# Performance work log

Hardware: AMD Instinct MI355X
Metric: run time of the kernel (lower is better)

## Reference

```python
import jax, jax.numpy as jnp
import numpy as np

THRESHOLD = 1.0
DECAY = 0.9
SURR_SLOPE = 10.0

B, T, IN, HID, OUT = 1024, 16, 2312, 1024, 10


def setup_inputs() -> dict:
    key = jax.random.key(0)
    kx, kw1, kb1, kw2, kb2 = jax.random.split(key, 5)
    x = jax.random.normal(kx, (B, T, IN), dtype=jnp.float32)
    # PyTorch nn.Linear default init: U(-1/sqrt(fan_in), 1/sqrt(fan_in))
    lim1 = 1.0 / np.sqrt(IN)
    lim2 = 1.0 / np.sqrt(HID)
    W1 = jax.random.uniform(kw1, (HID, IN), jnp.float32, -lim1, lim1)
    b1 = jax.random.uniform(kb1, (HID,), jnp.float32, -lim1, lim1)
    W2 = jax.random.uniform(kw2, (OUT, HID), jnp.float32, -lim2, lim2)
    b2 = jax.random.uniform(kb2, (OUT,), jnp.float32, -lim2, lim2)
    return {"x": x, "W1": W1, "b1": b1, "W2": W2, "b2": b2}


def _lif_step(v, inp):
    # leaky integrate-and-fire with sigmoid surrogate spike
    v_new = DECAY * v + inp
    spike = jax.nn.sigmoid(SURR_SLOPE * (v_new - THRESHOLD))
    v_next = v_new * (1.0 - spike)
    return v_next, spike


def reference(x, W1, b1, W2, b2):
    # x: [B, T, IN] -> spikes: [B, T, OUT]
    Bn = x.shape[0]
    v1_0 = jnp.zeros((Bn, W1.shape[0]), x.dtype)
    v2_0 = jnp.zeros((Bn, W2.shape[0]), x.dtype)

    # Precompute the first linear over all time steps (batched GEMM).
    h_all = jnp.einsum('bti,hi->bth', x, W1) + b1  # [B, T, HID]

    def step(carry, h_t):
        v1, v2 = carry
        v1, s1 = _lif_step(v1, h_t)                 # [B, HID]
        o_t = s1 @ W2.T + b2                        # [B, OUT]
        v2, s2 = _lif_step(v2, o_t)
        return (v1, v2), s2

    h_tb = jnp.swapaxes(h_all, 0, 1)                # [T, B, HID]
    _, spikes = jax.lax.scan(step, (v1_0, v2_0), h_tb)
    return jnp.swapaxes(spikes, 0, 1)               # [B, T, OUT]
```

## Files before the change

### kernel.cpp

```cpp
#include <hip/hip_runtime.h>

typedef _Float16 half8  __attribute__((ext_vector_type(8)));
typedef _Float16 half4v __attribute__((ext_vector_type(4)));
typedef float    floatx4 __attribute__((ext_vector_type(4)));

#define K_DIM 2312
#define KP    2368
#define N_DIM 1024
#define M_DIM 16384
#define T_DIM 16
#define O_DIM 10
#define NKT   73
#define NT_OLD 73
#define LDP 40

__global__ __launch_bounds__(256) void cvt_f32_f16_pad(const float* __restrict__ src,
                                                       _Float16* __restrict__ dst) {
  int row = blockIdx.x;
  const float* s = src + (size_t)row * K_DIM;
  _Float16* d = dst + (size_t)row * KP;
  for (int c = threadIdx.x; c < 296; c += 256) {
    half8 o;
    if (c < 289) {
      floatx4 a = *(const floatx4*)(s + c * 8);
      floatx4 b = *(const floatx4*)(s + c * 8 + 4);
      #pragma unroll
      for (int e = 0; e < 4; ++e) { o[e] = (_Float16)a[e]; o[4 + e] = (_Float16)b[e]; }
    } else {
      o = half8{0, 0, 0, 0, 0, 0, 0, 0};
    }
    *(half8*)(d + c * 8) = o;
  }
}

__device__ __forceinline__ void gload16(const void* g, void* l) {
  __builtin_amdgcn_global_load_lds((const __attribute__((address_space(1))) void*)g,
                                   (__attribute__((address_space(3))) void*)l, 16, 0, 0);
}

#define VMCNT(n)  asm volatile("s_waitcnt vmcnt(" #n ")" ::: "memory")
#define SBAR      __builtin_amdgcn_sched_barrier(0)

__global__ __launch_bounds__(512, 2) void gemm_fused3(const float* __restrict__ X,
                                                      const _Float16* __restrict__ Bw,
                                                      const float* __restrict__ b1,
                                                      float* __restrict__ h) {
  __shared__ __align__(16) float    As[3][256 * 32];
  __shared__ __align__(16) _Float16 Bs[3][256 * 32];

  const int tid  = threadIdx.x;
  const int lane = tid & 63;
  const int w    = tid >> 6;
  const int wm   = (w >> 1) * 64;
  const int wn   = (w & 1) * 128;
  const int bm   = blockIdx.x & 63;
  const int bn   = blockIdx.x >> 6;
  const int m0   = bm * 256;
  const int n0   = bn * 256;

  const int rOffA = lane >> 3;
  const int gsrcA = (lane & 7) ^ (lane >> 3);
  const float* xaw = X + (size_t)(m0 + w * 32) * K_DIM;

  const int rlo  = lane >> 2;
  const int keyB = (rlo >> 1) & 3;
  const int cch  = (lane & 3) ^ keyB;
  const _Float16* bg = Bw + (size_t)(n0 + w * 32 + rlo) * KP + cch * 8;
  const int stbB = (w * 32) * 32;

  floatx4 acc[4][8];
  #pragma unroll
  for (int i = 0; i < 4; ++i)
    #pragma unroll
    for (int j = 0; j < 8; ++j)
      acc[i][j] = floatx4{0.f, 0.f, 0.f, 0.f};

  const int fr = lane & 15;
  const int q  = lane >> 4;
  const int rdsB = (q ^ ((fr >> 1) & 3)) * 8;
  int offB[8];
  #pragma unroll
  for (int j = 0; j < 8; ++j) offB[j] = (wn + j * 16 + fr) * 32 + rdsB;
  const int cA = fr & 7;
  int offA0[4], offA1[4];
  #pragma unroll
  for (int i = 0; i < 4; ++i) {
    const int rowA = wm + i * 16 + fr;
    offA0[i] = rowA * 32 + ((2 * q)     ^ cA) * 4;
    offA1[i] = rowA * 32 + ((2 * q + 1) ^ cA) * 4;
  }

  floatx4 fA[8];
  half8   bf[8];

#define STAGE(tk) do {                                                       \
    const int _s = (tk) % 3;                                                 \
    _Pragma("unroll")                                                        \
    for (int _d = 0; _d < 4; ++_d) {                                         \
      int _k = (tk) * 32 + gsrcA * 4;                                        \
      _k = _k > 2308 ? 2308 : _k;                                            \
      const float* _src = xaw + (size_t)(_d * 8 + rOffA) * K_DIM + _k;       \
      gload16(_src, &As[_s][(w * 32 + _d * 8) * 32]);                        \
    }                                                                        \
    gload16(bg + (tk) * 32,           &Bs[_s][stbB]);                        \
    gload16(bg + (tk) * 32 + 16 * KP, &Bs[_s][stbB + 16 * 32]);              \
  } while (0)

#define READF(tk) do {                                                       \
    const float*    _A = As[(tk) % 3];                                       \
    const _Float16* _B = Bs[(tk) % 3];                                       \
    _Pragma("unroll")                                                        \
    for (int _i = 0; _i < 4; ++_i) {                                         \
      fA[2 * _i]     = *(const floatx4*)(&_A[offA0[_i]]);                    \
      fA[2 * _i + 1] = *(const floatx4*)(&_A[offA1[_i]]);                    \
    }                                                                        \
    _Pragma("unroll")                                                        \
    for (int _j = 0; _j < 8; ++_j) bf[_j] = *(const half8*)(&_B[offB[_j]]);  \
  } while (0)

#define MFMA32 do {                                                          \
    __builtin_amdgcn_s_setprio(1);                                           \
    _Pragma("unroll")                                                        \
    for (int _i = 0; _i < 4; ++_i) {                                         \
      half8 _ah;                                                             \
      _Pragma("unroll")                                                      \
      for (int _e = 0; _e < 4; ++_e) {                                       \
        _ah[_e]     = (_Float16)fA[2 * _i][_e];                              \
        _ah[4 + _e] = (_Float16)fA[2 * _i + 1][_e];                          \
      }                                                                      \
      _Pragma("unroll")                                                      \
      for (int _j = 0; _j < 8; ++_j)                                         \
        acc[_i][_j] = __builtin_amdgcn_mfma_f32_16x16x32_f16(_ah, bf[_j], acc[_i][_j], 0, 0, 0); \
    }                                                                        \
    __builtin_amdgcn_s_setprio(0);                                           \
  } while (0)

  STAGE(0); STAGE(1);
  VMCNT(6); SBAR;
  __builtin_amdgcn_s_barrier(); SBAR;
  READF(0);

  for (int t = 0; t < NKT - 2; ++t) {
    STAGE(t + 2);
    VMCNT(6); SBAR;
    __builtin_amdgcn_s_barrier(); SBAR;
    MFMA32;
    READF(t + 1);
  }

  VMCNT(0); SBAR;
  __builtin_amdgcn_s_barrier(); SBAR;
  MFMA32;
  READF(NKT - 1);
  MFMA32;

#undef STAGE
#undef READF
#undef MFMA32

  const int cr = (lane >> 4) * 4;
  #pragma unroll
  for (int j = 0; j < 8; ++j) {
    int col = n0 + wn + j * 16 + fr;
    float bv = b1[col];
    #pragma unroll
    for (int i = 0; i < 4; ++i) {
      int rbase = m0 + wm + i * 16 + cr;
      #pragma unroll
      for (int e = 0; e < 4; ++e)
        h[(size_t)(rbase + e) * N_DIM + col] = acc[i][j][e] + bv;
    }
  }
}

__device__ __forceinline__ void stage_load(const float* __restrict__ x,
                                           const float* __restrict__ w,
                                           int m0, int n0, int k0, int tid,
                                           floatx4 (&ar)[4], floatx4 (&br)[4]) {
  int r = tid >> 3;
  int c = (tid & 7) * 4;
  bool ok = (k0 + c) < K_DIM;
  #pragma unroll
  for (int i = 0; i < 4; ++i) {
    int row = r + 32 * i;
    if (ok) {
      ar[i] = *(const floatx4*)(x + (size_t)(m0 + row) * K_DIM + k0 + c);
      br[i] = *(const floatx4*)(w + (size_t)(n0 + row) * K_DIM + k0 + c);
    } else {
      ar[i] = floatx4{0.f, 0.f, 0.f, 0.f};
      br[i] = floatx4{0.f, 0.f, 0.f, 0.f};
    }
  }
}

__device__ __forceinline__ void stage_write(_Float16* __restrict__ Ab,
                                            _Float16* __restrict__ Bb, int tid,
                                            const floatx4 (&ar)[4], const floatx4 (&br)[4]) {
  int r = tid >> 3;
  int c = (tid & 7) * 4;
  #pragma unroll
  for (int i = 0; i < 4; ++i) {
    int row = r + 32 * i;
    half4v av, bv;
    #pragma unroll
    for (int e = 0; e < 4; ++e) {
      av[e] = (_Float16)ar[i][e];
      bv[e] = (_Float16)br[i][e];
    }
    *(half4v*)(Ab + row * LDP + c) = av;
    *(half4v*)(Bb + row * LDP + c) = bv;
  }
}

__global__ __launch_bounds__(256) void gemm1_kernel(const float* __restrict__ x,
                                                    const float* __restrict__ W1,
                                                    const float* __restrict__ b1,
                                                    float* __restrict__ h) {
  __shared__ _Float16 Al[2][128 * LDP];
  __shared__ _Float16 Bl[2][128 * LDP];

  int tid  = threadIdx.x;
  int lane = tid & 63;
  int w    = tid >> 6;
  int wm   = (w >> 1) * 64;
  int wn   = (w & 1) * 64;
  int m0   = (blockIdx.x >> 3) * 128;
  int n0   = (blockIdx.x & 7) * 128;

  floatx4 acc[4][4];
  #pragma unroll
  for (int i = 0; i < 4; ++i)
    #pragma unroll
    for (int j = 0; j < 4; ++j)
      acc[i][j] = floatx4{0.f, 0.f, 0.f, 0.f};

  floatx4 ar[4], br[4];
  stage_load(x, W1, m0, n0, 0, tid, ar, br);
  stage_write(Al[0], Bl[0], tid, ar, br);
  __syncthreads();

  int fr = lane & 15;
  int kc = (lane >> 4) * 8;

  int cur = 0;
  for (int kt = 0; kt < NT_OLD; ++kt) {
    if (kt + 1 < NT_OLD) stage_load(x, W1, m0, n0, (kt + 1) * 32, tid, ar, br);

    const _Float16* Ab = Al[cur];
    const _Float16* Bb = Bl[cur];
    half8 af[4], bf[4];
    #pragma unroll
    for (int f = 0; f < 4; ++f) {
      af[f] = *(const half8*)(Ab + (wm + f * 16 + fr) * LDP + kc);
      bf[f] = *(const half8*)(Bb + (wn + f * 16 + fr) * LDP + kc);
    }
    #pragma unroll
    for (int i = 0; i < 4; ++i)
      #pragma unroll
      for (int j = 0; j < 4; ++j)
        acc[i][j] = __builtin_amdgcn_mfma_f32_16x16x32_f16(af[i], bf[j], acc[i][j], 0, 0, 0);

    if (kt + 1 < NT_OLD) stage_write(Al[cur ^ 1], Bl[cur ^ 1], tid, ar, br);
    __syncthreads();
    cur ^= 1;
  }

  int cr = (lane >> 4) * 4;
  #pragma unroll
  for (int j = 0; j < 4; ++j) {
    int col = n0 + wn + j * 16 + fr;
    float bv = b1[col];
    #pragma unroll
    for (int i = 0; i < 4; ++i) {
      int rbase = m0 + wm + i * 16 + cr;
      #pragma unroll
      for (int e = 0; e < 4; ++e)
        h[(size_t)(rbase + e) * N_DIM + col] = acc[i][j][e] + bv;
    }
  }
}

__global__ __launch_bounds__(256) void snn_temporal_kernel(const float* __restrict__ h,
                                                           const float* __restrict__ W2,
                                                           const float* __restrict__ b2,
                                                           float* __restrict__ out) {
  __shared__ float w2s[O_DIM * N_DIM];
  int tid = threadIdx.x;
  for (int i = tid; i < O_DIM * N_DIM; i += 256) w2s[i] = W2[i];
  __syncthreads();

  int wave = tid >> 6;
  int lane = tid & 63;
  int b = blockIdx.x * 4 + wave;
  const float* hrow = h + (size_t)b * (T_DIM * N_DIM);
  float* orow = out + (size_t)b * (T_DIM * O_DIM);

  float v1[16];
  #pragma unroll
  for (int e = 0; e < 16; ++e) v1[e] = 0.f;
  float v2 = 0.f;
  float bias2 = (lane < O_DIM) ? b2[lane] : 0.f;

  floatx4 hv[4];
  #pragma unroll
  for (int c = 0; c < 4; ++c) hv[c] = *(const floatx4*)(hrow + c * 256 + lane * 4);

  for (int t = 0; t < T_DIM; ++t) {
    floatx4 hn[4];
    if (t + 1 < T_DIM) {
      #pragma unroll
      for (int c = 0; c < 4; ++c)
        hn[c] = *(const floatx4*)(hrow + (t + 1) * N_DIM + c * 256 + lane * 4);
    }

    float sarr[16];
    #pragma unroll
    for (int c = 0; c < 4; ++c) {
      #pragma unroll
      for (int e = 0; e < 4; ++e) {
        int ii = c * 4 + e;
        float vn = 0.9f * v1[ii] + hv[c][e];
        float s  = 1.f / (1.f + __expf(10.f - 10.f * vn));
        v1[ii] = vn * (1.f - s);
        sarr[ii] = s;
      }
    }

    float part[10];
    #pragma unroll
    for (int o = 0; o < O_DIM; ++o) {
      float a = 0.f;
      #pragma unroll
      for (int c = 0; c < 4; ++c) {
        floatx4 w4 = *(const floatx4*)&w2s[o * N_DIM + c * 256 + lane * 4];
        a += sarr[c * 4 + 0] * w4[0] + sarr[c * 4 + 1] * w4[1]
           + sarr[c * 4 + 2] * w4[2] + sarr[c * 4 + 3] * w4[3];
      }
      part[o] = a;
    }
    #pragma unroll
    for (int m = 1; m < 64; m <<= 1) {
      #pragma unroll
      for (int o = 0; o < O_DIM; ++o) part[o] += __shfl_xor(part[o], m, 64);
    }

    float po = part[0];
    #pragma unroll
    for (int o = 1; o < O_DIM; ++o) po = (lane == o) ? part[o] : po;

    if (lane < O_DIM) {
      float vo = 0.9f * v2 + po + bias2;
      float s2 = 1.f / (1.f + __expf(10.f - 10.f * vo));
      v2 = vo * (1.f - s2);
      orow[t * O_DIM + lane] = s2;
    }

    #pragma unroll
    for (int c = 0; c < 4; ++c) hv[c] = hn[c];
  }
}

extern "C" void kernel_launch(void* const* d_in, const int* in_sizes, int n_in,
                              void* d_out, int out_size, void* d_ws, size_t ws_size,
                              hipStream_t stream) {
  const float* x  = (const float*)d_in[0];
  const float* W1 = (const float*)d_in[1];
  const float* b1 = (const float*)d_in[2];
  const float* W2 = (const float*)d_in[3];
  const float* b2 = (const float*)d_in[4];
  float* out = (float*)d_out;

  float* h = (float*)d_ws;

  const size_t H_BYTES  = (size_t)M_DIM * N_DIM * 4;
  const size_t WH_BYTES = (size_t)N_DIM * KP * 2;
  const size_t NEED = H_BYTES + WH_BYTES;

  if (ws_size >= NEED) {
    _Float16* w1h = (_Float16*)((char*)d_ws + H_BYTES);
    cvt_f32_f16_pad<<<dim3(N_DIM), dim3(256), 0, stream>>>(W1, w1h);
    gemm_fused3<<<dim3(256), dim3(512), 0, stream>>>(x, w1h, b1, h);
  } else {
    gemm1_kernel<<<dim3(1024), dim3(256), 0, stream>>>(x, W1, b1, h);
  }
  snn_temporal_kernel<<<dim3(256), dim3(256), 0, stream>>>(h, W2, b2, out);
}
```

Baseline: 132.4 us.

## Split GEMM main loop into quadrant phases interleaving DMA, LDS reads and MFMA

Restructures the fused fp32xfp16 GEMM main loop into four sub-phases per K tile. Each phase reads part of the A/B fragments from LDS, issues part of the next-next tile's global-to-LDS loads, and runs a quarter of the MFMAs, with barriers in between (ping-pong style). It also changes the A-tile LDS swizzle and global load mapping. The aim is finer interleaving of memory traffic with matrix work. The cost is many more barriers per iteration, which may add synchronisation overhead.

```diff
diff --git a/kernel.cpp b/kernel.cpp
--- a/kernel.cpp
+++ b/kernel.cpp
@@ -39,9 +39,11 @@
 }
 
 #define VMCNT(n)  asm volatile("s_waitcnt vmcnt(" #n ")" ::: "memory")
+#define LGKM0     asm volatile("s_waitcnt lgkmcnt(0)" ::: "memory")
 #define SBAR      __builtin_amdgcn_sched_barrier(0)
-
-__global__ __launch_bounds__(512, 2) void gemm_fused3(const float* __restrict__ X,
+#define BARRIER   __builtin_amdgcn_s_barrier()
+
+__global__ __launch_bounds__(512, 2) void gemm_fused4(const float* __restrict__ X,
                                                       const _Float16* __restrict__ Bw,
                                                       const float* __restrict__ b1,
                                                       float* __restrict__ h) {
@@ -58,13 +60,16 @@
   const int m0   = bm * 256;
   const int n0   = bn * 256;
 
-  const int rOffA = lane >> 3;
-  const int gsrcA = (lane & 7) ^ (lane >> 3);
-  const float* xaw = X + (size_t)(m0 + w * 32) * K_DIM;
-
   const int rlo  = lane >> 2;
+  const int l2   = lane & 3;
+  const int hpA  = (rlo & 1) * 16 + (l2 ^ ((rlo >> 1) & 3)) * 4;
+  const float* xrow[4];
+  #pragma unroll
+  for (int d = 0; d < 4; ++d)
+    xrow[d] = X + (size_t)(m0 + w * 32 + d * 8 + (rlo >> 1)) * K_DIM;
+
   const int keyB = (rlo >> 1) & 3;
-  const int cch  = (lane & 3) ^ keyB;
+  const int cch  = l2 ^ keyB;
   const _Float16* bg = Bw + (size_t)(n0 + w * 32 + rlo) * KP + cch * 8;
   const int stbB = (w * 32) * 32;
 
@@ -81,82 +86,86 @@
   int offB[8];
   #pragma unroll
   for (int j = 0; j < 8; ++j) offB[j] = (wn + j * 16 + fr) * 32 + rdsB;
-  const int cA = fr & 7;
-  int offA0[4], offA1[4];
+  int offA[8];
   #pragma unroll
   for (int i = 0; i < 4; ++i) {
     const int rowA = wm + i * 16 + fr;
-    offA0[i] = rowA * 32 + ((2 * q)     ^ cA) * 4;
-    offA1[i] = rowA * 32 + ((2 * q + 1) ^ cA) * 4;
+    #pragma unroll
+    for (int e = 0; e < 2; ++e)
+      offA[2 * i + e] = rowA * 32 + (q >> 1) * 16 + ((2 * (q & 1) + e) ^ (rowA & 3)) * 4;
   }
 
   floatx4 fA[8];
   half8   bf[8];
 
-#define STAGE(tk) do {                                                       \
-    const int _s = (tk) % 3;                                                 \
+#define DMA_A(tk, d) do {                                                    \
+    int _kk = (tk) * 32 + hpA; _kk = _kk > 2308 ? 2308 : _kk;                \
+    gload16(xrow[d] + _kk, &As[(tk) % 3][(w * 4 + (d)) * 256]);              \
+  } while (0)
+#define DMA_B(tk, half) do {                                                 \
+    gload16(bg + (tk) * 32 + (half) * 16 * KP,                               \
+            &Bs[(tk) % 3][stbB + (half) * 16 * 32]);                         \
+  } while (0)
+#define RD_A(tk, ih) do { const float* _A = As[(tk) % 3];                    \
+    fA[4*(ih)+0] = *(const floatx4*)(&_A[offA[4*(ih)+0]]);                   \
+    fA[4*(ih)+1] = *(const floatx4*)(&_A[offA[4*(ih)+1]]);                   \
+    fA[4*(ih)+2] = *(const floatx4*)(&_A[offA[4*(ih)+2]]);                   \
+    fA[4*(ih)+3] = *(const floatx4*)(&_A[offA[4*(ih)+3]]); } while (0)
+#define RD_B(tk, jh) do { const _Float16* _B = Bs[(tk) % 3];                 \
     _Pragma("unroll")                                                        \
-    for (int _d = 0; _d < 4; ++_d) {                                         \
-      int _k = (tk) * 32 + gsrcA * 4;                                        \
-      _k = _k > 2308 ? 2308 : _k;                                            \
-      const float* _src = xaw + (size_t)(_d * 8 + rOffA) * K_DIM + _k;       \
-      gload16(_src, &As[_s][(w * 32 + _d * 8) * 32]);                        \
-    }                                                                        \
-    gload16(bg + (tk) * 32,           &Bs[_s][stbB]);                        \
-    gload16(bg + (tk) * 32 + 16 * KP, &Bs[_s][stbB + 16 * 32]);              \
-  } while (0)
-
-#define READF(tk) do {                                                       \
-    const float*    _A = As[(tk) % 3];                                       \
-    const _Float16* _B = Bs[(tk) % 3];                                       \
-    _Pragma("unroll")                                                        \
-    for (int _i = 0; _i < 4; ++_i) {                                         \
-      fA[2 * _i]     = *(const floatx4*)(&_A[offA0[_i]]);                    \
-      fA[2 * _i + 1] = *(const floatx4*)(&_A[offA1[_i]]);                    \
-    }                                                                        \
-    _Pragma("unroll")                                                        \
-    for (int _j = 0; _j < 8; ++_j) bf[_j] = *(const half8*)(&_B[offB[_j]]);  \
-  } while (0)
-
-#define MFMA32 do {                                                          \
+    for (int _j = 0; _j < 4; ++_j)                                           \
+      bf[4*(jh)+_j] = *(const half8*)(&_B[offB[4*(jh)+_j]]); } while (0)
+#define MQ(ih, jh) do {                                                      \
     __builtin_amdgcn_s_setprio(1);                                           \
     _Pragma("unroll")                                                        \
-    for (int _i = 0; _i < 4; ++_i) {                                         \
+    for (int _i = 2*(ih); _i < 2*(ih)+2; ++_i) {                             \
       half8 _ah;                                                             \
       _Pragma("unroll")                                                      \
       for (int _e = 0; _e < 4; ++_e) {                                       \
-        _ah[_e]     = (_Float16)fA[2 * _i][_e];                              \
-        _ah[4 + _e] = (_Float16)fA[2 * _i + 1][_e];                          \
+        _ah[_e]     = (_Float16)fA[2*_i][_e];                                \
+        _ah[4+_e]   = (_Float16)fA[2*_i+1][_e];                              \
       }                                                                      \
       _Pragma("unroll")                                                      \
-      for (int _j = 0; _j < 8; ++_j)                                         \
+      for (int _j = 4*(jh); _j < 4*(jh)+4; ++_j)                             \
         acc[_i][_j] = __builtin_amdgcn_mfma_f32_16x16x32_f16(_ah, bf[_j], acc[_i][_j], 0, 0, 0); \
     }                                                                        \
     __builtin_amdgcn_s_setprio(0);                                           \
   } while (0)
 
-  STAGE(0); STAGE(1);
+  DMA_A(0,0); DMA_A(0,1); DMA_A(0,2); DMA_A(0,3); DMA_B(0,0); DMA_B(0,1);
+  DMA_A(1,0); DMA_A(1,1); DMA_A(1,2); DMA_A(1,3); DMA_B(1,0); DMA_B(1,1);
   VMCNT(6); SBAR;
-  __builtin_amdgcn_s_barrier(); SBAR;
-  READF(0);
-
-  for (int t = 0; t < NKT - 2; ++t) {
-    STAGE(t + 2);
-    VMCNT(6); SBAR;
-    __builtin_amdgcn_s_barrier(); SBAR;
-    MFMA32;
-    READF(t + 1);
-  }
-
-  VMCNT(0); SBAR;
-  __builtin_amdgcn_s_barrier(); SBAR;
-  MFMA32;
-  READF(NKT - 1);
-  MFMA32;
-
-#undef STAGE
-#undef READF
-#undef MFMA32
+  BARRIER; SBAR;
+
+  for (int t = 0; t < NKT; ++t) {
+    const bool st = (t + 2 < NKT);
+    RD_A(t, 0); RD_B(t, 0);
+    if (st) { DMA_A(t + 2, 0); DMA_A(t + 2, 1); }
+    BARRIER; LGKM0; SBAR;
+    MQ(0, 0);
+    BARRIER; SBAR;
+    RD_B(t, 1);
+    if (st) { DMA_A(t + 2, 2); DMA_A(t + 2, 3); }
+    BARRIER; LGKM0; SBAR;
+    MQ(0, 1);
+    BARRIER; SBAR;
+    RD_A(t, 1);
+    if (st) { DMA_B(t + 2, 0); DMA_B(t + 2, 1); }
+    BARRIER; LGKM0; SBAR;
+    MQ(1, 1);
+    BARRIER; SBAR;
+    if (st) { VMCNT(6); } else { VMCNT(0); }
+    SBAR;
+    BARRIER; SBAR;
+    MQ(1, 0);
+    BARRIER; SBAR;
+  }
+
+#undef DMA_A
+#undef DMA_B
+#undef RD_A
+#undef RD_B
+#undef MQ
 
   const int cr = (lane >> 4) * 4;
   #pragma unroll
@@ -379,7 +388,7 @@
   if (ws_size >= NEED) {
     _Float16* w1h = (_Float16*)((char*)d_ws + H_BYTES);
     cvt_f32_f16_pad<<<dim3(N_DIM), dim3(256), 0, stream>>>(W1, w1h);
-    gemm_fused3<<<dim3(256), dim3(512), 0, stream>>>(x, w1h, b1, h);
+    gemm_fused4<<<dim3(256), dim3(512), 0, stream>>>(x, w1h, b1, h);
   } else {
     gemm1_kernel<<<dim3(1024), dim3(256), 0, stream>>>(x, W1, b1, h);
   }
```

Result: slower. 159.1 us (+20.1%).

## Fuse layer-1 LIF recurrence into GEMM epilogue and emit fp16 spikes

Applied to the files above, without the earlier changes.

The layer-1 leaky integrate-and-fire recurrence now runs inside the GEMM epilogue. Each 256-row M tile holds 16 batch items by 16 timesteps, so the tile is staged through LDS and each thread walks the 16 timesteps for one batch item and column. Only fp16 spikes are written, not the fp32 hidden activations, which halves the intermediate write and lets a simpler layer-2 kernel read half the bytes. In exchange the epilogue gains extra barriers and LDS traffic, and spikes are rounded to fp16.

```diff
diff --git a/kernel.cpp b/kernel.cpp
--- a/kernel.cpp
+++ b/kernel.cpp
@@ -41,10 +41,10 @@
 #define VMCNT(n)  asm volatile("s_waitcnt vmcnt(" #n ")" ::: "memory")
 #define SBAR      __builtin_amdgcn_sched_barrier(0)
 
-__global__ __launch_bounds__(512, 2) void gemm_fused3(const float* __restrict__ X,
-                                                      const _Float16* __restrict__ Bw,
-                                                      const float* __restrict__ b1,
-                                                      float* __restrict__ h) {
+__global__ __launch_bounds__(512, 2) void gemm_lif1(const float* __restrict__ X,
+                                                    const _Float16* __restrict__ Bw,
+                                                    const float* __restrict__ b1,
+                                                    _Float16* __restrict__ s1) {
   __shared__ __align__(16) float    As[3][256 * 32];
   __shared__ __align__(16) _Float16 Bs[3][256 * 32];
 
@@ -158,18 +158,102 @@
 #undef READF
 #undef MFMA32
 
-  const int cr = (lane >> 4) * 4;
+  float* ch = (float*)As;
+  const int colIdx = (w & 1) * 16 + fr;
+  const int bloc = tid >> 5;
+  const int ci   = tid & 31;
+  const int gcolBase = n0 + (ci >> 4) * 128 + (ci & 15);
+
   #pragma unroll
   for (int j = 0; j < 8; ++j) {
-    int col = n0 + wn + j * 16 + fr;
-    float bv = b1[col];
+    __syncthreads();
     #pragma unroll
     for (int i = 0; i < 4; ++i) {
-      int rbase = m0 + wm + i * 16 + cr;
+      const int rl = wm + i * 16 + 4 * q;
       #pragma unroll
       for (int e = 0; e < 4; ++e)
-        h[(size_t)(rbase + e) * N_DIM + col] = acc[i][j][e] + bv;
-    }
+        ch[(rl + e) * 33 + colIdx] = acc[i][j][e];
+    }
+    __syncthreads();
+    const int gcol = gcolBase + j * 16;
+    const float bv = b1[gcol];
+    float hv[16];
+    #pragma unroll
+    for (int t = 0; t < 16; ++t) hv[t] = ch[(bloc * 16 + t) * 33 + ci];
+    float v = 0.f;
+    _Float16* srow = s1 + (size_t)(m0 + bloc * 16) * N_DIM + gcol;
+    #pragma unroll
+    for (int t = 0; t < 16; ++t) {
+      float vn = 0.9f * v + hv[t] + bv;
+      float s  = 1.f / (1.f + __expf(10.f - 10.f * vn));
+      v = vn * (1.f - s);
+      srow[(size_t)t * N_DIM] = (_Float16)s;
+    }
+  }
+}
+
+__global__ __launch_bounds__(256) void snn_layer2_kernel(const _Float16* __restrict__ s1,
+                                                         const float* __restrict__ W2,
+                                                         const float* __restrict__ b2,
+                                                         float* __restrict__ out) {
+  __shared__ float w2s[O_DIM * N_DIM];
+  int tid = threadIdx.x;
+  for (int i = tid; i < O_DIM * N_DIM; i += 256) w2s[i] = W2[i];
+  __syncthreads();
+
+  int wave = tid >> 6;
+  int lane = tid & 63;
+  int b = blockIdx.x * 4 + wave;
+  const _Float16* srow = s1 + (size_t)b * (T_DIM * N_DIM) + lane * 16;
+  float* orow = out + (size_t)b * (T_DIM * O_DIM);
+
+  float v2 = 0.f;
+  float bias2 = (lane < O_DIM) ? b2[lane] : 0.f;
+
+  half8 p0 = *(const half8*)(srow);
+  half8 p1 = *(const half8*)(srow + 8);
+
+  for (int t = 0; t < T_DIM; ++t) {
+    half8 n0h, n1h;
+    if (t + 1 < T_DIM) {
+      n0h = *(const half8*)(srow + (t + 1) * N_DIM);
+      n1h = *(const half8*)(srow + (t + 1) * N_DIM + 8);
+    }
+
+    float sv[16];
+    #pragma unroll
+    for (int e = 0; e < 8; ++e) { sv[e] = (float)p0[e]; sv[8 + e] = (float)p1[e]; }
+
+    float part[O_DIM];
+    #pragma unroll
+    for (int o = 0; o < O_DIM; ++o) {
+      float a = 0.f;
+      #pragma unroll
+      for (int c = 0; c < 4; ++c) {
+        floatx4 w4 = *(const floatx4*)&w2s[o * N_DIM + lane * 16 + c * 4];
+        a += sv[c * 4 + 0] * w4[0] + sv[c * 4 + 1] * w4[1]
+           + sv[c * 4 + 2] * w4[2] + sv[c * 4 + 3] * w4[3];
+      }
+      part[o] = a;
+    }
+    #pragma unroll
+    for (int m = 1; m < 64; m <<= 1) {
+      #pragma unroll
+      for (int o = 0; o < O_DIM; ++o) part[o] += __shfl_xor(part[o], m, 64);
+    }
+
+    float po = part[0];
+    #pragma unroll
+    for (int o = 1; o < O_DIM; ++o) po = (lane == o) ? part[o] : po;
+
+    if (lane < O_DIM) {
+      float vo = 0.9f * v2 + po + bias2;
+      float s2 = 1.f / (1.f + __expf(10.f - 10.f * vo));
+      v2 = vo * (1.f - s2);
+      orow[t * O_DIM + lane] = s2;
+    }
+
+    p0 = n0h; p1 = n1h;
   }
 }
 
@@ -370,18 +454,19 @@
   const float* b2 = (const float*)d_in[4];
   float* out = (float*)d_out;
 
-  float* h = (float*)d_ws;
-
-  const size_t H_BYTES  = (size_t)M_DIM * N_DIM * 4;
+  const size_t S1_BYTES = (size_t)M_DIM * N_DIM * 2;
   const size_t WH_BYTES = (size_t)N_DIM * KP * 2;
-  const size_t NEED = H_BYTES + WH_BYTES;
+  const size_t NEED = S1_BYTES + WH_BYTES;
 
   if (ws_size >= NEED) {
-    _Float16* w1h = (_Float16*)((char*)d_ws + H_BYTES);
+    _Float16* s1h = (_Float16*)d_ws;
+    _Float16* w1h = (_Float16*)((char*)d_ws + S1_BYTES);
     cvt_f32_f16_pad<<<dim3(N_DIM), dim3(256), 0, stream>>>(W1, w1h);
-    gemm_fused3<<<dim3(256), dim3(512), 0, stream>>>(x, w1h, b1, h);
+    gemm_lif1<<<dim3(256), dim3(512), 0, stream>>>(x, w1h, b1, s1h);
+    snn_layer2_kernel<<<dim3(256), dim3(256), 0, stream>>>(s1h, W2, b2, out);
   } else {
+    float* h = (float*)d_ws;
     gemm1_kernel<<<dim3(1024), dim3(256), 0, stream>>>(x, W1, b1, h);
-  }
-  snn_temporal_kernel<<<dim3(256), dim3(256), 0, stream>>>(h, W2, b2, out);
-}
+    snn_temporal_kernel<<<dim3(256), dim3(256), 0, stream>>>(h, W2, b2, out);
+  }
+}
```

Result: faster. 128.7 us, median of 3 (-2.8%).
